# Kernel optimization log

Measured on AMD Instinct MI355X. Metric: run time of the kernel, lower is better.

Reference implementation:

```python
import jax, jax.numpy as jnp
import numpy as np

TOP_K = 2  # routing_method: renormalize top-2 (topk then softmax over selected logits)


def setup_inputs() -> dict:
    key = jax.random.key(0)
    ks = jax.random.split(key, 5)
    T, H, I, E = 4096, 1024, 4096, 8
    return {
        "hidden_states": jax.random.normal(ks[0], (T, H), jnp.float32),
        "router_logits": jax.random.normal(ks[1], (T, E), jnp.float32),
        "W_gate": jax.random.normal(ks[2], (E, H, I), jnp.float32) * 0.02,  # w1
        "W_up": jax.random.normal(ks[3], (E, H, I), jnp.float32) * 0.02,   # w3
        "W_down": jax.random.normal(ks[4], (E, I, H), jnp.float32) * 0.02, # w2
    }


def reference(hidden_states, router_logits, W_gate, W_up, W_down):
    # Routing: top-k logits, renormalize with softmax over selected logits.
    top_vals, top_idx = jax.lax.top_k(router_logits, TOP_K)        # [T, K]
    routing_weights = jax.nn.softmax(top_vals, axis=-1)            # [T, K]

    E = W_gate.shape[0]
    out = jnp.zeros_like(hidden_states)                            # [T, H]
    for e in range(E):  # fixed small expert loop (structurally distinct weights)
        # combine weight for expert e per token (0 if not routed here)
        w_e = jnp.sum(jnp.where(top_idx == e, routing_weights, 0.0), axis=-1)  # [T]
        gate = hidden_states @ W_gate[e]                           # [T, I]
        up = hidden_states @ W_up[e]                               # [T, I]
        y = (jax.nn.silu(gate) * up) @ W_down[e]                   # [T, H]
        out = out + w_e[:, None] * y
    return out
```

## Files before the change

### kernel.cpp

```cpp
#include <hip/hip_runtime.h>

typedef float    f32x4 __attribute__((ext_vector_type(4)));
typedef _Float16 f16x8 __attribute__((ext_vector_type(8)));
typedef _Float16 f16x4 __attribute__((ext_vector_type(4)));

#define T_TOK 4096
#define HD    1024
#define ID    4096
#define NE    8
#define TOTP  (2*T_TOK)
#define MAXT1 72
#define MAXT2 40

#define WS_CNT   0
#define WS_FILL  64
#define WS_OFF   128
#define WS_TOT   192
#define WS_TOT2  196
#define WS_TEXP  256
#define WS_TM0   (256 + 4*MAXT1)
#define WS_TEXP2 (256 + 8*MAXT1)
#define WS_TM02  (256 + 8*MAXT1 + 4*MAXT2)
#define WS_TOPE  2048
#define WS_TOPW  (WS_TOPE + 4*TOTP)
#define WS_PAIR  (WS_TOPW + 4*TOTP)
#define WS_ACT   ((size_t)1 << 20)
constexpr size_t WS_YBUF = WS_ACT  + 2ull*TOTP*ID;
constexpr size_t WS_HS16 = WS_YBUF + 2ull*TOTP*HD;
constexpr size_t WS_WG16 = WS_HS16 + 2ull*T_TOK*HD;
constexpr size_t WS_WU16 = WS_WG16 + 2ull*NE*HD*ID;
constexpr size_t WS_WD16 = WS_WU16 + 2ull*NE*HD*ID;
constexpr size_t WS_YB0  = WS_WG16;
constexpr size_t WS_YB1  = WS_WG16 + 2ull*TOTP*HD;

__device__ __forceinline__ void gll16(const void* g, void* l) {
  __builtin_amdgcn_global_load_lds(
      (const __attribute__((address_space(1))) unsigned int*)g,
      (__attribute__((address_space(3))) unsigned int*)l, 16, 0, 0);
}

#define WAITV(N) do { \
    asm volatile("s_waitcnt vmcnt(" #N ")" ::: "memory"); \
    __builtin_amdgcn_sched_barrier(0); \
  } while (0)

__device__ __forceinline__ int lofs(int row, int g) {
  return row * 32 + ((g ^ ((row >> 1) & 3)) << 3);
}

__global__ void k_router(const float* __restrict__ logits, char* __restrict__ ws) {
  int t = blockIdx.x * blockDim.x + threadIdx.x;
  if (t >= T_TOK) return;
  float v0 = -1e30f, v1 = -1e30f; int i0 = 0, i1 = 0;
  #pragma unroll
  for (int e = 0; e < NE; ++e) {
    float v = logits[t * NE + e];
    if (v > v0)      { v1 = v0; i1 = i0; v0 = v; i0 = e; }
    else if (v > v1) { v1 = v;  i1 = e; }
  }
  float w0 = 1.f / (1.f + __expf(v1 - v0));
  ((int*)(ws + WS_TOPE))[2*t]   = i0;
  ((int*)(ws + WS_TOPE))[2*t+1] = i1;
  ((float*)(ws + WS_TOPW))[2*t]   = w0;
  ((float*)(ws + WS_TOPW))[2*t+1] = 1.f - w0;
  atomicAdd(&((int*)(ws + WS_CNT))[i0], 1);
  atomicAdd(&((int*)(ws + WS_CNT))[i1], 1);
}

__global__ void k_prefix(char* __restrict__ ws) {
  if (threadIdx.x != 0 || blockIdx.x != 0) return;
  const int* cnt = (const int*)(ws + WS_CNT);
  int* off   = (int*)(ws + WS_OFF);
  int* texp  = (int*)(ws + WS_TEXP);
  int* tm0   = (int*)(ws + WS_TM0);
  int* texp2 = (int*)(ws + WS_TEXP2);
  int* tm02  = (int*)(ws + WS_TM02);
  int run = 0, t1 = 0, t2 = 0;
  for (int e = 0; e < NE; ++e) {
    off[e] = run;
    int ne = cnt[e];
    for (int i = 0; i < ne; i += 128) { texp[t1] = e; tm0[t1] = i; ++t1; }
    for (int i = 0; i < ne; i += 256) { texp2[t2] = e; tm02[t2] = i; ++t2; }
    run += ne;
  }
  off[NE] = run;
  *(int*)(ws + WS_TOT)  = t1;
  *(int*)(ws + WS_TOT2) = t2;
}

__global__ void k_scatter(char* __restrict__ ws) {
  int t = blockIdx.x * blockDim.x + threadIdx.x;
  if (t >= T_TOK) return;
  const int* tope = (const int*)(ws + WS_TOPE);
  const int* off  = (const int*)(ws + WS_OFF);
  int* fill = (int*)(ws + WS_FILL);
  int* pair = (int*)(ws + WS_PAIR);
  #pragma unroll
  for (int s = 0; s < 2; ++s) {
    int id = 2*t + s;
    int e = tope[id];
    int pos = off[e] + atomicAdd(&fill[e], 1);
    pair[pos] = id;
  }
}

__global__ void k_hscvt(const float* __restrict__ src, _Float16* __restrict__ dst) {
  int i = blockIdx.x * blockDim.x + threadIdx.x;
  f32x4 v = ((const f32x4*)src)[i];
  f16x4 o;
  #pragma unroll
  for (int j = 0; j < 4; ++j) o[j] = (_Float16)v[j];
  ((f16x4*)dst)[i] = o;
}

__global__ __launch_bounds__(256) void k_wtrans(const float* __restrict__ src,
                                                _Float16* __restrict__ dst,
                                                int K, int N) {
  const int e = blockIdx.z;
  const int n0 = blockIdx.x * 64, k0 = blockIdx.y * 64;
  const float* s = src + (size_t)e * K * N;
  _Float16* d = dst + (size_t)e * (size_t)K * N;
  __shared__ _Float16 t[64][68];
  const int tx = threadIdx.x & 15, ty = threadIdx.x >> 4;
  #pragma unroll
  for (int it = 0; it < 4; ++it) {
    int k = k0 + it*16 + ty;
    f32x4 v = *(const f32x4*)&s[(size_t)k * N + n0 + tx*4];
    #pragma unroll
    for (int j = 0; j < 4; ++j) t[tx*4 + j][it*16 + ty] = (_Float16)v[j];
  }
  __syncthreads();
  #pragma unroll
  for (int it = 0; it < 4; ++it) {
    int n = it*16 + ty;
    *(f16x4*)&d[(size_t)(n0 + n) * K + k0 + tx*4] = *(const f16x4*)&t[n][tx*4];
  }
}

#define G1_BUF 16384
__global__ __launch_bounds__(512, 2) void k_gemm1(
    const _Float16* __restrict__ hs16, const _Float16* __restrict__ WgT,
    const _Float16* __restrict__ WuT, char* __restrict__ ws) {
  const int s = blockIdx.y;
  if (s >= *(const int*)(ws + WS_TOT2)) return;
  const int e    = ((const int*)(ws + WS_TEXP2))[s];
  const int m0   = ((const int*)(ws + WS_TM02))[s];
  const int offE = ((const int*)(ws + WS_OFF))[e];
  const int nE   = ((const int*)(ws + WS_CNT))[e];
  _Float16* __restrict__ act = (_Float16*)(ws + WS_ACT);
  const int n0 = blockIdx.x * 128;
  const int tid = threadIdx.x, lane = tid & 63, wid = tid >> 6;

  __shared__ __align__(16) _Float16 sm[4 * G1_BUF];

  const int rL = lane >> 2;
  const int q  = (((lane & 3) ^ ((lane >> 3) & 3)) << 3);
  const int* __restrict__ pairp = (const int*)(ws + WS_PAIR);
  const _Float16 *aP[2], *gP, *uP;
  #pragma unroll
  for (int c = 0; c < 2; ++c) {
    int mm = m0 + 32*wid + 16*c + rL;
    int tok = (mm < nE) ? (pairp[offE + mm] >> 1) : 0;
    aP[c] = hs16 + (size_t)tok * HD + q;
  }
  {
    size_t col = (size_t)e * ID + (n0 + 16*wid + rL);
    gP = WgT + col * HD + q;
    uP = WuT + col * HD + q;
  }

  auto stage = [&](int buf, int kt) {
    _Float16* b = sm + buf * G1_BUF;
    const int ko = kt * 32;
    gll16(aP[0] + ko, b + (32*wid) * 32);
    gll16(aP[1] + ko, b + (32*wid + 16) * 32);
    gll16(gP + ko, b + 8192  + (16*wid) * 32);
    gll16(uP + ko, b + 12288 + (16*wid) * 32);
  };

  const int wr = wid >> 2, wc = wid & 3;
  const int l15 = lane & 15, l4 = lane >> 4;
  f32x4 accg[8][2] = {}, accu[8][2] = {};

  auto compute = [&](int buf) {
    const _Float16* b0 = sm + buf * G1_BUF;
    f16x8 afr[8], bg[2], bu[2];
    #pragma unroll
    for (int i = 0; i < 8; ++i)
      afr[i] = *(const f16x8*)&b0[lofs(128*wr + 16*i + l15, l4)];
    #pragma unroll
    for (int j = 0; j < 2; ++j) {
      bg[j] = *(const f16x8*)&b0[8192  + lofs(32*wc + 16*j + l15, l4)];
      bu[j] = *(const f16x8*)&b0[12288 + lofs(32*wc + 16*j + l15, l4)];
    }
    __builtin_amdgcn_s_setprio(1);
    #pragma unroll
    for (int i = 0; i < 8; ++i)
      #pragma unroll
      for (int j = 0; j < 2; ++j) {
        accg[i][j] = __builtin_amdgcn_mfma_f32_16x16x32_f16(afr[i], bg[j], accg[i][j], 0, 0, 0);
        accu[i][j] = __builtin_amdgcn_mfma_f32_16x16x32_f16(afr[i], bu[j], accu[i][j], 0, 0, 0);
      }
    __builtin_amdgcn_s_setprio(0);
  };

  const int KT = HD / 32;
  stage(0, 0); stage(1, 1); stage(2, 2);
  for (int t = 0; t < KT - 3; ++t) {
    stage((t + 3) & 3, t + 3);
    WAITV(12);
    __builtin_amdgcn_s_barrier();
    compute(t & 3);
    __builtin_amdgcn_s_barrier();
  }
  WAITV(8);
  __builtin_amdgcn_s_barrier();
  compute((KT - 3) & 3);
  __builtin_amdgcn_s_barrier();
  WAITV(4);
  __builtin_amdgcn_s_barrier();
  compute((KT - 2) & 3);
  __builtin_amdgcn_s_barrier();
  WAITV(0);
  __builtin_amdgcn_s_barrier();
  compute((KT - 1) & 3);

  #pragma unroll
  for (int i = 0; i < 8; ++i)
    #pragma unroll
    for (int r = 0; r < 4; ++r) {
      const int mm = m0 + 128*wr + 16*i + 4*l4 + r;
      if (mm < nE) {
        const size_t prow = (size_t)(offE + mm) * ID;
        #pragma unroll
        for (int j = 0; j < 2; ++j) {
          float g = accg[i][j][r], u = accu[i][j][r];
          float sv = g / (1.f + __expf(-g)) * u;
          act[prow + n0 + 32*wc + 16*j + l15] = (_Float16)sv;
        }
      }
    }
}

#define G2_BUF 12288
__global__ __launch_bounds__(256, 2) void k_gemm2(const _Float16* __restrict__ WdT,
                                                  char* __restrict__ ws) {
  const int s = blockIdx.y;
  if (s >= *(const int*)(ws + WS_TOT)) return;
  const int e    = ((const int*)(ws + WS_TEXP))[s];
  const int m0   = ((const int*)(ws + WS_TM0))[s];
  const int offE = ((const int*)(ws + WS_OFF))[e];
  const int nE   = ((const int*)(ws + WS_CNT))[e];
  const int h    = blockIdx.z;
  const int kbase = h * (ID / 2);
  const int* __restrict__ pair = (const int*)(ws + WS_PAIR);
  const _Float16* __restrict__ act = (const _Float16*)(ws + WS_ACT);
  _Float16* __restrict__ yb = (_Float16*)(ws + (h ? WS_YB1 : WS_YB0));
  const int n0 = blockIdx.x * 256;
  const int tid = threadIdx.x, lane = tid & 63, wid = tid >> 6;

  __shared__ __align__(16) _Float16 sm[3 * G2_BUF];

  const int rL = lane >> 2;
  const int q  = (((lane & 3) ^ ((lane >> 3) & 3)) << 3);
  const _Float16 *aS[2], *bS[4];
  #pragma unroll
  for (int c = 0; c < 2; ++c) {
    int mm = m0 + 32*wid + 16*c + rL;
    int p = (mm < nE) ? (offE + mm) : offE;
    aS[c] = act + (size_t)p * ID + kbase + q;
  }
  #pragma unroll
  for (int c = 0; c < 4; ++c)
    bS[c] = WdT + ((size_t)e * HD + (n0 + 64*wid + 16*c + rL)) * ID + kbase + q;

  auto stage = [&](int buf, int kt) {
    _Float16* b = sm + buf * G2_BUF;
    const int ko = kt * 32;
    #pragma unroll
    for (int c = 0; c < 2; ++c) gll16(aS[c] + ko, b + (32*wid + 16*c) * 32);
    #pragma unroll
    for (int c = 0; c < 4; ++c) gll16(bS[c] + ko, b + 4096 + (64*wid + 16*c) * 32);
  };

  const int wr = wid >> 1, wc = wid & 1;
  const int l15 = lane & 15, l4 = lane >> 4;
  f32x4 acc[4][8] = {};

  auto compute = [&](int buf) {
    const _Float16* b0 = sm + buf * G2_BUF;
    f16x8 afr[4], bfr[8];
    #pragma unroll
    for (int i = 0; i < 4; ++i)
      afr[i] = *(const f16x8*)&b0[lofs(64*wr + 16*i + l15, l4)];
    #pragma unroll
    for (int j = 0; j < 8; ++j)
      bfr[j] = *(const f16x8*)&b0[4096 + lofs(128*wc + 16*j + l15, l4)];
    __builtin_amdgcn_s_setprio(1);
    #pragma unroll
    for (int i = 0; i < 4; ++i)
      #pragma unroll
      for (int j = 0; j < 8; ++j)
        acc[i][j] = __builtin_amdgcn_mfma_f32_16x16x32_f16(afr[i], bfr[j], acc[i][j], 0, 0, 0);
    __builtin_amdgcn_s_setprio(0);
  };

  const int KT = (ID / 2) / 32;
  stage(0, 0); stage(1, 1);
  for (int t = 0; t < KT - 2; ++t) {
    stage((t + 2) % 3, t + 2);
    WAITV(12);
    __builtin_amdgcn_s_barrier();
    compute(t % 3);
    __builtin_amdgcn_s_barrier();
  }
  WAITV(6);
  __builtin_amdgcn_s_barrier();
  compute((KT - 2) % 3);
  __builtin_amdgcn_s_barrier();
  WAITV(0);
  __builtin_amdgcn_s_barrier();
  compute((KT - 1) % 3);

  #pragma unroll
  for (int i = 0; i < 4; ++i)
    #pragma unroll
    for (int r = 0; r < 4; ++r) {
      const int mm = m0 + 64*wr + 16*i + 4*l4 + r;
      if (mm < nE) {
        const int id = pair[offE + mm];
        #pragma unroll
        for (int j = 0; j < 8; ++j)
          yb[(size_t)id * HD + n0 + 128*wc + 16*j + l15] = (_Float16)acc[i][j][r];
      }
    }
}

__global__ void k_combine(const char* __restrict__ ws, float* __restrict__ out) {
  const int idx = blockIdx.x * blockDim.x + threadIdx.x;
  const int t = idx >> 7, c = idx & 127;
  const float* topw = (const float*)(ws + WS_TOPW);
  const _Float16* y0p = (const _Float16*)(ws + WS_YB0);
  const _Float16* y1p = (const _Float16*)(ws + WS_YB1);
  f16x8 a0 = ((const f16x8*)(y0p + (size_t)(2*t)     * HD))[c];
  f16x8 b0 = ((const f16x8*)(y1p + (size_t)(2*t)     * HD))[c];
  f16x8 a1 = ((const f16x8*)(y0p + (size_t)(2*t + 1) * HD))[c];
  f16x8 b1 = ((const f16x8*)(y1p + (size_t)(2*t + 1) * HD))[c];
  const float w0 = topw[2*t], w1 = topw[2*t+1];
  f32x4 o0, o1;
  #pragma unroll
  for (int j = 0; j < 4; ++j) {
    o0[j] = w0 * ((float)a0[j]     + (float)b0[j])     + w1 * ((float)a1[j]     + (float)b1[j]);
    o1[j] = w0 * ((float)a0[4 + j] + (float)b0[4 + j]) + w1 * ((float)a1[4 + j] + (float)b1[4 + j]);
  }
  ((f32x4*)out)[2*idx]     = o0;
  ((f32x4*)out)[2*idx + 1] = o1;
}

extern "C" void kernel_launch(void* const* d_in, const int* in_sizes, int n_in,
                              void* d_out, int out_size, void* d_ws, size_t ws_size,
                              hipStream_t stream) {
  const float* hs     = (const float*)d_in[0];
  const float* logits = (const float*)d_in[1];
  const float* Wg     = (const float*)d_in[2];
  const float* Wu     = (const float*)d_in[3];
  const float* Wd     = (const float*)d_in[4];
  char* ws = (char*)d_ws;

  _Float16* hs16 = (_Float16*)(ws + WS_HS16);
  _Float16* wg16 = (_Float16*)(ws + WS_WG16);
  _Float16* wu16 = (_Float16*)(ws + WS_WU16);
  _Float16* wd16 = (_Float16*)(ws + WS_WD16);

  hipMemsetAsync(ws, 0, 256, stream);
  k_router <<<dim3(T_TOK/256), dim3(256), 0, stream>>>(logits, ws);
  k_prefix <<<dim3(1),         dim3(64),  0, stream>>>(ws);
  k_scatter<<<dim3(T_TOK/256), dim3(256), 0, stream>>>(ws);
  k_hscvt  <<<dim3(T_TOK*HD/4/256), dim3(256), 0, stream>>>(hs, hs16);
  k_wtrans <<<dim3(ID/64, HD/64, NE), dim3(256), 0, stream>>>(Wg, wg16, HD, ID);
  k_wtrans <<<dim3(ID/64, HD/64, NE), dim3(256), 0, stream>>>(Wu, wu16, HD, ID);
  k_wtrans <<<dim3(HD/64, ID/64, NE), dim3(256), 0, stream>>>(Wd, wd16, ID, HD);
  k_gemm1  <<<dim3(ID/128, MAXT2),    dim3(512), 0, stream>>>(hs16, wg16, wu16, ws);
  k_gemm2  <<<dim3(HD/256, MAXT1, 2), dim3(256), 0, stream>>>(wd16, ws);
  k_combine<<<dim3(T_TOK*HD/8/256), dim3(256), 0, stream>>>(ws, (float*)d_out);
}
```

Baseline: 486.5 us.

## Split gate/up GEMM K-step into two half-phases interleaving LDS reads, loads and MFMA

Restructures the main loop of the gate/up GEMM kernel so each K-step runs as two halves. Each half reads part of the A fragments from LDS, issues half of the next stage's global-to-LDS loads, then runs its MFMA group between barriers. The aim is to overlap LDS reads and global loads with matrix math and to cut register pressure by holding four A fragments instead of eight. It adds more barriers and lgkmcnt waits per K-step, which may cost synchronisation overhead.

```diff
diff --git a/kernel.cpp b/kernel.cpp
--- a/kernel.cpp
+++ b/kernel.cpp
@@ -44,6 +44,11 @@
     __builtin_amdgcn_sched_barrier(0); \
   } while (0)
 
+#define LGKM0 do { \
+    asm volatile("s_waitcnt lgkmcnt(0)" ::: "memory"); \
+    __builtin_amdgcn_sched_barrier(0); \
+  } while (0)
+
 __device__ __forceinline__ int lofs(int row, int g) {
   return row * 32 + ((g ^ ((row >> 1) & 3)) << 3);
 }
@@ -169,11 +174,15 @@
     uP = WuT + col * HD + q;
   }
 
-  auto stage = [&](int buf, int kt) {
+  auto stA = [&](int buf, int kt) {
     _Float16* b = sm + buf * G1_BUF;
     const int ko = kt * 32;
     gll16(aP[0] + ko, b + (32*wid) * 32);
     gll16(aP[1] + ko, b + (32*wid + 16) * 32);
+  };
+  auto stB = [&](int buf, int kt) {
+    _Float16* b = sm + buf * G1_BUF;
+    const int ko = kt * 32;
     gll16(gP + ko, b + 8192  + (16*wid) * 32);
     gll16(uP + ko, b + 12288 + (16*wid) * 32);
   };
@@ -181,49 +190,66 @@
   const int wr = wid >> 2, wc = wid & 3;
   const int l15 = lane & 15, l4 = lane >> 4;
   f32x4 accg[8][2] = {}, accu[8][2] = {};
-
-  auto compute = [&](int buf) {
+  f16x8 afr[4], bg[2], bu[2];
+
+  auto rd0 = [&](int buf) {
     const _Float16* b0 = sm + buf * G1_BUF;
-    f16x8 afr[8], bg[2], bu[2];
-    #pragma unroll
-    for (int i = 0; i < 8; ++i)
+    #pragma unroll
+    for (int i = 0; i < 4; ++i)
       afr[i] = *(const f16x8*)&b0[lofs(128*wr + 16*i + l15, l4)];
     #pragma unroll
     for (int j = 0; j < 2; ++j) {
       bg[j] = *(const f16x8*)&b0[8192  + lofs(32*wc + 16*j + l15, l4)];
       bu[j] = *(const f16x8*)&b0[12288 + lofs(32*wc + 16*j + l15, l4)];
     }
+  };
+  auto rd1 = [&](int buf) {
+    const _Float16* b0 = sm + buf * G1_BUF;
+    #pragma unroll
+    for (int i = 0; i < 4; ++i)
+      afr[i] = *(const f16x8*)&b0[lofs(128*wr + 64 + 16*i + l15, l4)];
+  };
+  auto fma0 = [&]() {
+    __builtin_amdgcn_s_barrier();
+    LGKM0;
     __builtin_amdgcn_s_setprio(1);
     #pragma unroll
-    for (int i = 0; i < 8; ++i)
+    for (int i = 0; i < 4; ++i)
       #pragma unroll
       for (int j = 0; j < 2; ++j) {
         accg[i][j] = __builtin_amdgcn_mfma_f32_16x16x32_f16(afr[i], bg[j], accg[i][j], 0, 0, 0);
         accu[i][j] = __builtin_amdgcn_mfma_f32_16x16x32_f16(afr[i], bu[j], accu[i][j], 0, 0, 0);
       }
     __builtin_amdgcn_s_setprio(0);
+    __builtin_amdgcn_s_barrier();
+  };
+  auto fma1 = [&]() {
+    __builtin_amdgcn_s_barrier();
+    LGKM0;
+    __builtin_amdgcn_s_setprio(1);
+    #pragma unroll
+    for (int i = 0; i < 4; ++i)
+      #pragma unroll
+      for (int j = 0; j < 2; ++j) {
+        accg[4+i][j] = __builtin_amdgcn_mfma_f32_16x16x32_f16(afr[i], bg[j], accg[4+i][j], 0, 0, 0);
+        accu[4+i][j] = __builtin_amdgcn_mfma_f32_16x16x32_f16(afr[i], bu[j], accu[4+i][j], 0, 0, 0);
+      }
+    __builtin_amdgcn_s_setprio(0);
+    __builtin_amdgcn_s_barrier();
   };
 
   const int KT = HD / 32;
-  stage(0, 0); stage(1, 1); stage(2, 2);
-  for (int t = 0; t < KT - 3; ++t) {
-    stage((t + 3) & 3, t + 3);
-    WAITV(12);
-    __builtin_amdgcn_s_barrier();
-    compute(t & 3);
-    __builtin_amdgcn_s_barrier();
-  }
+  stA(0, 0); stB(0, 0); stA(1, 1); stB(1, 1); stA(2, 2); stB(2, 2);
   WAITV(8);
   __builtin_amdgcn_s_barrier();
-  compute((KT - 3) & 3);
-  __builtin_amdgcn_s_barrier();
-  WAITV(4);
-  __builtin_amdgcn_s_barrier();
-  compute((KT - 2) & 3);
-  __builtin_amdgcn_s_barrier();
-  WAITV(0);
-  __builtin_amdgcn_s_barrier();
-  compute((KT - 1) & 3);
+  for (int t = 0; t < KT - 3; ++t) {
+    const int buf = t & 3, nb = (t + 3) & 3;
+    rd0(buf); stA(nb, t + 3); fma0();
+    rd1(buf); stB(nb, t + 3); WAITV(8); fma1();
+  }
+  rd0((KT-3) & 3); fma0(); rd1((KT-3) & 3); WAITV(4); fma1();
+  rd0((KT-2) & 3); fma0(); rd1((KT-2) & 3); WAITV(0); fma1();
+  rd0((KT-1) & 3); fma0(); rd1((KT-1) & 3); fma1();
 
   #pragma unroll
   for (int i = 0; i < 8; ++i)
```

After: 482.2 us. About the same (-0.9%).
